# Performance work log

Hardware: AMD Instinct MI355X
Metric: run time of the kernel (lower is better)

The kernel has to match this reference:

```python
import jax, jax.numpy as jnp
import numpy as np

TEMPERATURE = 1.0
EXAGGERATION = 1.0


def setup_inputs() -> dict:
    key = jax.random.key(0)
    features = jax.random.normal(key, (8192, 128), dtype=jnp.float32)
    return {"features": features}


def _cauchy_sim(x, y):
    # 1 / ((cdist(x,y) * t)^2 + 1) == 1 / (t^2 * sq_dist + 1)
    sq = (
        jnp.sum(x * x, axis=1)[:, None]
        + jnp.sum(y * y, axis=1)[None, :]
        - 2.0 * (x @ y.T)
    )
    sq = jnp.maximum(sq, 0.0)  # numerical floor, matches cdist >= 0
    return 1.0 / (sq * (TEMPERATURE * TEMPERATURE) + 1.0)


def reference(features):
    batch_size = features.shape[0] // 2
    a = features[:batch_size]
    b = features[batch_size:]

    sim_aa = _cauchy_sim(a, a)  # [B, B]
    sim_bb = _cauchy_sim(b, b)  # [B, B]
    sim_ab = _cauchy_sim(a, b)  # [B, B]

    tempered_alignment = jnp.mean(jnp.log(jnp.diagonal(sim_ab)))

    self_mask = jnp.eye(batch_size, dtype=bool)
    sim_aa = jnp.where(self_mask, 0.0, sim_aa)
    sim_bb = jnp.where(self_mask, 0.0, sim_bb)

    # hstack((sim_ab.T, sim_bb)).sum(1) == sim_ab.sum(0) + sim_bb.sum(1)
    logsumexp_1 = jnp.mean(jnp.log(jnp.sum(sim_ab, axis=0) + jnp.sum(sim_bb, axis=1)))
    logsumexp_2 = jnp.mean(jnp.log(jnp.sum(sim_aa, axis=1) + jnp.sum(sim_ab, axis=1)))
    raw_uniformity = logsumexp_1 + logsumexp_2

    loss = -(EXAGGERATION * tempered_alignment - raw_uniformity / 2.0)
    return loss
```

## Files before the change

kernel.cpp:

```cpp
#include <hip/hip_runtime.h>
#include <hip/hip_bf16.h>

typedef __bf16 bf16x8 __attribute__((ext_vector_type(8)));
typedef float  f32x4  __attribute__((ext_vector_type(4)));

static constexpr int D      = 128;
static constexpr int BATCH  = 4096;
static constexpr int N      = 8192;
static constexpr int BT     = 256;
static constexpr int NT     = N / BT;
static constexpr int TRI    = NT * (NT + 1) / 2;

__device__ __forceinline__ void load_lds16(const void* g, void* l) {
    __builtin_amdgcn_global_load_lds(
        (const __attribute__((address_space(1))) unsigned int*)g,
        (__attribute__((address_space(3))) unsigned int*)l, 16, 0, 0);
}

__global__ __launch_bounds__(256) void prep_kernel(const float* __restrict__ f,
                                                   unsigned short* __restrict__ fb,
                                                   float* __restrict__ norms,
                                                   float* __restrict__ out) {
    if (blockIdx.x == 0 && threadIdx.x == 0) out[0] = 0.f;
    const int w = threadIdx.x >> 6, lane = threadIdx.x & 63;
    const int row = blockIdx.x * 4 + w;
    const float2 v = *(const float2*)(f + (size_t)row * D + lane * 2);
    union { __bf16 h[2]; unsigned int u; } pk;
    pk.h[0] = (__bf16)v.x; pk.h[1] = (__bf16)v.y;
    *(unsigned int*)(fb + (size_t)row * D + lane * 2) = pk.u;
    float s = v.x * v.x + v.y * v.y;
    #pragma unroll
    for (int m = 1; m <= 32; m <<= 1) s += __shfl_xor(s, m);
    if (lane == 0) norms[row] = s;
}

__global__ __launch_bounds__(512) void sim_kernel(const unsigned short* __restrict__ fbf,
                                                  const float* __restrict__ norms,
                                                  float* __restrict__ Prow,
                                                  float* __restrict__ diag) {
    int id = blockIdx.x;
    int ti = (int)((sqrtf(8.f * (float)id + 1.f) - 1.f) * 0.5f);
    while ((ti + 1) * (ti + 2) / 2 <= id) ++ti;
    while (ti * (ti + 1) / 2 > id) --ti;
    const int tj = id - ti * (ti + 1) / 2;
    const bool diagblk = (ti == tj);

    __shared__ __align__(16) unsigned char AsB[BT * 128];
    __shared__ __align__(16) unsigned char BsB[BT * 128];
    __shared__ float rowbuf[256];
    __shared__ float colbuf[256];

    const int tid = threadIdx.x;
    if (tid < 256) rowbuf[tid] = 0.f;
    else           colbuf[tid - 256] = 0.f;

    const int wv = tid >> 6, lane = tid & 63;
    const int lr = lane & 15, hk = lane >> 4;
    const int qr = (wv >> 2) * 128;
    const int qc = (wv & 3) * 64;

    const unsigned char* Abase = (const unsigned char*)fbf + (size_t)ti * BT * 256;
    const unsigned char* Bbase = (const unsigned char*)fbf + (size_t)tj * BT * 256;
    const unsigned char* Brd = diagblk ? AsB : BsB;

    f32x4 acc[8][4];
    #pragma unroll
    for (int i = 0; i < 8; ++i)
        #pragma unroll
        for (int j = 0; j < 4; ++j)
            acc[i][j] = (f32x4){0.f, 0.f, 0.f, 0.f};

    #pragma unroll
    for (int kp = 0; kp < 2; ++kp) {
        if (kp) __syncthreads();
        #pragma unroll
        for (int it = 0; it < 4; ++it) {
            const int cid = it * 512 + tid;
            const int row = cid >> 3, p = cid & 7;
            const int sw = ((p ^ (row & 7)) << 4);
            load_lds16(Abase + (size_t)row * 256 + kp * 128 + sw,
                       AsB + it * 8192 + wv * 1024);
        }
        if (!diagblk) {
            #pragma unroll
            for (int it = 0; it < 4; ++it) {
                const int cid = it * 512 + tid;
                const int row = cid >> 3, p = cid & 7;
                const int sw = ((p ^ (row & 7)) << 4);
                load_lds16(Bbase + (size_t)row * 256 + kp * 128 + sw,
                           BsB + it * 8192 + wv * 1024);
            }
        }
        __syncthreads();

        #pragma unroll
        for (int l = 0; l < 2; ++l) {
            const int c = l * 4 + hk;
            bf16x8 av[8], bv[4];
            #pragma unroll
            for (int fi = 0; fi < 8; ++fi) {
                const int row = qr + fi * 16 + lr;
                av[fi] = *(const bf16x8*)(AsB + row * 128 + ((c ^ (row & 7)) << 4));
            }
            #pragma unroll
            for (int fj = 0; fj < 4; ++fj) {
                const int row = qc + fj * 16 + lr;
                bv[fj] = *(const bf16x8*)(Brd + row * 128 + ((c ^ (row & 7)) << 4));
            }
            #pragma unroll
            for (int fi = 0; fi < 8; ++fi)
                #pragma unroll
                for (int fj = 0; fj < 4; ++fj)
                    acc[fi][fj] = __builtin_amdgcn_mfma_f32_16x16x32_bf16(av[fi], bv[fj], acc[fi][fj], 0, 0, 0);
        }
    }

    float colN[4];
    #pragma unroll
    for (int fj = 0; fj < 4; ++fj)
        colN[fj] = norms[tj * BT + qc + fj * 16 + lr];

    const int colBase = tj * BT;
    const bool stripe = (ti == tj + 16);

    #pragma unroll
    for (int fi = 0; fi < 8; ++fi) {
        const int irow = qr + fi * 16 + hk * 4;
        float rowN[4];
        #pragma unroll
        for (int r = 0; r < 4; ++r)
            rowN[r] = norms[ti * BT + irow + r];
        #pragma unroll
        for (int fj = 0; fj < 4; ++fj) {
            const int icol = qc + fj * 16 + lr;
            #pragma unroll
            for (int r = 0; r < 4; ++r) {
                float sq = rowN[r] + colN[fj] - 2.f * acc[fi][fj][r];
                sq = fmaxf(sq, 0.f);
                float sim = __builtin_amdgcn_rcpf(sq + 1.f);
                if (diagblk && (irow + r == icol)) sim = 0.f;
                if (stripe && (irow + r == icol)) diag[colBase + icol] = sim;
                acc[fi][fj][r] = sim;
            }
        }
    }

    #pragma unroll
    for (int fi = 0; fi < 8; ++fi) {
        float rs[4];
        #pragma unroll
        for (int r = 0; r < 4; ++r)
            rs[r] = acc[fi][0][r] + acc[fi][1][r] + acc[fi][2][r] + acc[fi][3][r];
        #pragma unroll
        for (int r = 0; r < 4; ++r) {
            rs[r] += __shfl_xor(rs[r], 1);
            rs[r] += __shfl_xor(rs[r], 2);
            rs[r] += __shfl_xor(rs[r], 4);
            rs[r] += __shfl_xor(rs[r], 8);
        }
        if (lr == 0) {
            #pragma unroll
            for (int r = 0; r < 4; ++r)
                atomicAdd(&rowbuf[qr + fi * 16 + hk * 4 + r], rs[r]);
        }
    }

    if (!diagblk) {
        #pragma unroll
        for (int fj = 0; fj < 4; ++fj) {
            float cs = 0.f;
            #pragma unroll
            for (int fi = 0; fi < 8; ++fi)
                #pragma unroll
                for (int r = 0; r < 4; ++r)
                    cs += acc[fi][fj][r];
            cs += __shfl_xor(cs, 16);
            cs += __shfl_xor(cs, 32);
            if (hk == 0)
                atomicAdd(&colbuf[qc + fj * 16 + lr], cs);
        }
    }
    __syncthreads();

    float* PR = Prow + ((size_t)ti * NT + tj) * BT;
    float* PC = Prow + ((size_t)tj * NT + ti) * BT;
    if (tid < 256) {
        PR[tid] = rowbuf[tid];
        if (!diagblk) PC[tid] = colbuf[tid];
    }
}

__global__ __launch_bounds__(256) void finalize_kernel(const float* __restrict__ Prow,
                                                       const float* __restrict__ diag,
                                                       float* __restrict__ out) {
    const int ti = blockIdx.x;
    const int r  = threadIdx.x;
    const float* base = Prow + (size_t)ti * NT * BT + r;
    float s = 0.f;
    #pragma unroll
    for (int k = 0; k < NT; ++k) s += base[k * BT];
    const int i = ti * BT + r;
    float term = 0.5f * __logf(s);
    if (i >= BATCH) term -= __logf(diag[i - BATCH]);
    #pragma unroll
    for (int m = 1; m <= 32; m <<= 1) term += __shfl_xor(term, m);
    __shared__ float sh[4];
    if ((threadIdx.x & 63) == 0) sh[threadIdx.x >> 6] = term;
    __syncthreads();
    if (threadIdx.x == 0)
        atomicAdd(out, (sh[0] + sh[1] + sh[2] + sh[3]) / (float)BATCH);
}

extern "C" void kernel_launch(void* const* d_in, const int* in_sizes, int n_in,
                              void* d_out, int out_size, void* d_ws, size_t ws_size,
                              hipStream_t stream) {
    const float* feat = (const float*)d_in[0];
    char* ws = (char*)d_ws;
    unsigned short* fbf = (unsigned short*)ws;
    float* norms = (float*)(ws + (2u << 20));
    float* diag  = (float*)(ws + (2u << 20) + 32768);
    float* Prow  = (float*)(ws + (2u << 20) + 49152);
    float* out   = (float*)d_out;

    prep_kernel<<<N / 4, 256, 0, stream>>>(feat, fbf, norms, out);
    sim_kernel<<<TRI, 512, 0, stream>>>(fbf, norms, Prow, diag);
    finalize_kernel<<<NT, 256, 0, stream>>>(Prow, diag, out);
}
```

Before: 90.42 us.

## Replace LDS-tiled 256x256 blocks with single-wave 64x64 register tiles

The sim kernel now has one 64-lane wave per 64x64 triangular tile. Each wave loads its bf16 fragments straight from global memory into registers, so the LDS staging, barriers and shared-memory atomics are gone. Row and column partial sums are written directly to a workspace laid out so that finalize only reads the populated slots. This gives far more, smaller blocks (8256 instead of 528) for load balance and latency hiding, but each tile reuses less data and global/L2 traffic grows.

```diff
diff --git a/kernel.cpp b/kernel.cpp
--- a/kernel.cpp
+++ b/kernel.cpp
@@ -4,18 +4,12 @@
 typedef __bf16 bf16x8 __attribute__((ext_vector_type(8)));
 typedef float  f32x4  __attribute__((ext_vector_type(4)));
 
-static constexpr int D      = 128;
-static constexpr int BATCH  = 4096;
-static constexpr int N      = 8192;
-static constexpr int BT     = 256;
-static constexpr int NT     = N / BT;
-static constexpr int TRI    = NT * (NT + 1) / 2;
-
-__device__ __forceinline__ void load_lds16(const void* g, void* l) {
-    __builtin_amdgcn_global_load_lds(
-        (const __attribute__((address_space(1))) unsigned int*)g,
-        (__attribute__((address_space(3))) unsigned int*)l, 16, 0, 0);
-}
+static constexpr int D     = 128;
+static constexpr int BATCH = 4096;
+static constexpr int N     = 8192;
+static constexpr int WT    = 64;
+static constexpr int NT    = N / WT;
+static constexpr int TRI   = NT * (NT + 1) / 2;
 
 __global__ __launch_bounds__(256) void prep_kernel(const float* __restrict__ f,
                                                    unsigned short* __restrict__ fb,
@@ -34,120 +28,80 @@
     if (lane == 0) norms[row] = s;
 }
 
-__global__ __launch_bounds__(512) void sim_kernel(const unsigned short* __restrict__ fbf,
-                                                  const float* __restrict__ norms,
-                                                  float* __restrict__ Prow,
-                                                  float* __restrict__ diag) {
-    int id = blockIdx.x;
+__global__ __launch_bounds__(64, 3) void wave_kernel(const unsigned short* __restrict__ fbf,
+                                                     const float* __restrict__ norms,
+                                                     float* __restrict__ Prow,
+                                                     float* __restrict__ diag) {
+    const int id = blockIdx.x;
     int ti = (int)((sqrtf(8.f * (float)id + 1.f) - 1.f) * 0.5f);
     while ((ti + 1) * (ti + 2) / 2 <= id) ++ti;
     while (ti * (ti + 1) / 2 > id) --ti;
     const int tj = id - ti * (ti + 1) / 2;
     const bool diagblk = (ti == tj);
+    const bool stripe  = (ti == tj + 64);
 
-    __shared__ __align__(16) unsigned char AsB[BT * 128];
-    __shared__ __align__(16) unsigned char BsB[BT * 128];
-    __shared__ float rowbuf[256];
-    __shared__ float colbuf[256];
+    const int lane = threadIdx.x;
+    const int lr = lane & 15, hk = lane >> 4;
 
-    const int tid = threadIdx.x;
-    if (tid < 256) rowbuf[tid] = 0.f;
-    else           colbuf[tid - 256] = 0.f;
+    const unsigned char* Ab = (const unsigned char*)fbf + (size_t)ti * WT * 256;
+    const unsigned char* Bb = (const unsigned char*)fbf + (size_t)tj * WT * 256;
 
-    const int wv = tid >> 6, lane = tid & 63;
-    const int lr = lane & 15, hk = lane >> 4;
-    const int qr = (wv >> 2) * 128;
-    const int qc = (wv & 3) * 64;
-
-    const unsigned char* Abase = (const unsigned char*)fbf + (size_t)ti * BT * 256;
-    const unsigned char* Bbase = (const unsigned char*)fbf + (size_t)tj * BT * 256;
-    const unsigned char* Brd = diagblk ? AsB : BsB;
-
-    f32x4 acc[8][4];
+    f32x4 acc[4][4];
     #pragma unroll
-    for (int i = 0; i < 8; ++i)
+    for (int i = 0; i < 4; ++i)
         #pragma unroll
         for (int j = 0; j < 4; ++j)
             acc[i][j] = (f32x4){0.f, 0.f, 0.f, 0.f};
 
     #pragma unroll
-    for (int kp = 0; kp < 2; ++kp) {
-        if (kp) __syncthreads();
+    for (int ks = 0; ks < 4; ++ks) {
+        const int ko = (ks * 4 + hk) * 16;
+        bf16x8 av[4], bv[4];
         #pragma unroll
-        for (int it = 0; it < 4; ++it) {
-            const int cid = it * 512 + tid;
-            const int row = cid >> 3, p = cid & 7;
-            const int sw = ((p ^ (row & 7)) << 4);
-            load_lds16(Abase + (size_t)row * 256 + kp * 128 + sw,
-                       AsB + it * 8192 + wv * 1024);
-        }
-        if (!diagblk) {
+        for (int fi = 0; fi < 4; ++fi)
+            av[fi] = *(const bf16x8*)(Ab + (fi * 16 + lr) * 256 + ko);
+        #pragma unroll
+        for (int fj = 0; fj < 4; ++fj)
+            bv[fj] = *(const bf16x8*)(Bb + (fj * 16 + lr) * 256 + ko);
+        #pragma unroll
+        for (int fi = 0; fi < 4; ++fi)
             #pragma unroll
-            for (int it = 0; it < 4; ++it) {
-                const int cid = it * 512 + tid;
-                const int row = cid >> 3, p = cid & 7;
-                const int sw = ((p ^ (row & 7)) << 4);
-                load_lds16(Bbase + (size_t)row * 256 + kp * 128 + sw,
-                           BsB + it * 8192 + wv * 1024);
-            }
-        }
-        __syncthreads();
-
-        #pragma unroll
-        for (int l = 0; l < 2; ++l) {
-            const int c = l * 4 + hk;
-            bf16x8 av[8], bv[4];
-            #pragma unroll
-            for (int fi = 0; fi < 8; ++fi) {
-                const int row = qr + fi * 16 + lr;
-                av[fi] = *(const bf16x8*)(AsB + row * 128 + ((c ^ (row & 7)) << 4));
-            }
-            #pragma unroll
-            for (int fj = 0; fj < 4; ++fj) {
-                const int row = qc + fj * 16 + lr;
-                bv[fj] = *(const bf16x8*)(Brd + row * 128 + ((c ^ (row & 7)) << 4));
-            }
-            #pragma unroll
-            for (int fi = 0; fi < 8; ++fi)
-                #pragma unroll
-                for (int fj = 0; fj < 4; ++fj)
-                    acc[fi][fj] = __builtin_amdgcn_mfma_f32_16x16x32_bf16(av[fi], bv[fj], acc[fi][fj], 0, 0, 0);
-        }
+            for (int fj = 0; fj < 4; ++fj)
+                acc[fi][fj] = __builtin_amdgcn_mfma_f32_16x16x32_bf16(av[fi], bv[fj], acc[fi][fj], 0, 0, 0);
     }
 
-    float colN[4];
+    float rowN[4][4], colN[4];
+    #pragma unroll
+    for (int fi = 0; fi < 4; ++fi)
+        #pragma unroll
+        for (int r = 0; r < 4; ++r)
+            rowN[fi][r] = norms[ti * WT + fi * 16 + hk * 4 + r];
     #pragma unroll
     for (int fj = 0; fj < 4; ++fj)
-        colN[fj] = norms[tj * BT + qc + fj * 16 + lr];
-
-    const int colBase = tj * BT;
-    const bool stripe = (ti == tj + 16);
+        colN[fj] = norms[tj * WT + fj * 16 + lr];
 
     #pragma unroll
-    for (int fi = 0; fi < 8; ++fi) {
-        const int irow = qr + fi * 16 + hk * 4;
-        float rowN[4];
-        #pragma unroll
-        for (int r = 0; r < 4; ++r)
-            rowN[r] = norms[ti * BT + irow + r];
+    for (int fi = 0; fi < 4; ++fi) {
+        const int lrow = fi * 16 + hk * 4;
         #pragma unroll
         for (int fj = 0; fj < 4; ++fj) {
-            const int icol = qc + fj * 16 + lr;
+            const int lcol = fj * 16 + lr;
             #pragma unroll
             for (int r = 0; r < 4; ++r) {
-                float sq = rowN[r] + colN[fj] - 2.f * acc[fi][fj][r];
+                float sq = rowN[fi][r] + colN[fj] - 2.f * acc[fi][fj][r];
                 sq = fmaxf(sq, 0.f);
                 float sim = __builtin_amdgcn_rcpf(sq + 1.f);
-                if (diagblk && (irow + r == icol)) sim = 0.f;
-                if (stripe && (irow + r == icol)) diag[colBase + icol] = sim;
+                if (diagblk && (lrow + r == lcol)) sim = 0.f;
+                if (stripe && (lrow + r == lcol)) diag[tj * WT + lcol] = sim;
                 acc[fi][fj][r] = sim;
             }
         }
     }
 
+    float* PR = Prow + ((size_t)ti * 256 + tj) * WT;
     #pragma unroll
-    for (int fi = 0; fi < 8; ++fi) {
-        float rs[4];
+    for (int fi = 0; fi < 4; ++fi) {
+        f32x4 rs;
         #pragma unroll
         for (int r = 0; r < 4; ++r)
             rs[r] = acc[fi][0][r] + acc[fi][1][r] + acc[fi][2][r] + acc[fi][3][r];
@@ -158,57 +112,44 @@
             rs[r] += __shfl_xor(rs[r], 4);
             rs[r] += __shfl_xor(rs[r], 8);
         }
-        if (lr == 0) {
-            #pragma unroll
-            for (int r = 0; r < 4; ++r)
-                atomicAdd(&rowbuf[qr + fi * 16 + hk * 4 + r], rs[r]);
-        }
+        if (lr == 0)
+            *(f32x4*)(PR + fi * 16 + hk * 4) = rs;
     }
 
     if (!diagblk) {
+        float* PC = Prow + ((size_t)tj * 256 + 128 + ti) * WT;
         #pragma unroll
         for (int fj = 0; fj < 4; ++fj) {
             float cs = 0.f;
             #pragma unroll
-            for (int fi = 0; fi < 8; ++fi)
+            for (int fi = 0; fi < 4; ++fi)
                 #pragma unroll
                 for (int r = 0; r < 4; ++r)
                     cs += acc[fi][fj][r];
             cs += __shfl_xor(cs, 16);
             cs += __shfl_xor(cs, 32);
             if (hk == 0)
-                atomicAdd(&colbuf[qc + fj * 16 + lr], cs);
+                PC[fj * 16 + lr] = cs;
         }
-    }
-    __syncthreads();
-
-    float* PR = Prow + ((size_t)ti * NT + tj) * BT;
-    float* PC = Prow + ((size_t)tj * NT + ti) * BT;
-    if (tid < 256) {
-        PR[tid] = rowbuf[tid];
-        if (!diagblk) PC[tid] = colbuf[tid];
     }
 }
 
-__global__ __launch_bounds__(256) void finalize_kernel(const float* __restrict__ Prow,
-                                                       const float* __restrict__ diag,
-                                                       float* __restrict__ out) {
-    const int ti = blockIdx.x;
-    const int r  = threadIdx.x;
-    const float* base = Prow + (size_t)ti * NT * BT + r;
+__global__ __launch_bounds__(64) void finalize_kernel(const float* __restrict__ Prow,
+                                                      const float* __restrict__ diag,
+                                                      float* __restrict__ out) {
+    const int t = blockIdx.x;
+    const int r = threadIdx.x;
+    const float* base = Prow + (size_t)t * 256 * WT + r;
     float s = 0.f;
-    #pragma unroll
-    for (int k = 0; k < NT; ++k) s += base[k * BT];
-    const int i = ti * BT + r;
+    for (int k = 0; k <= t; ++k)          s += base[k * WT];
+    for (int k = 129 + t; k < 256; ++k)   s += base[k * WT];
+    const int i = t * WT + r;
     float term = 0.5f * __logf(s);
     if (i >= BATCH) term -= __logf(diag[i - BATCH]);
     #pragma unroll
     for (int m = 1; m <= 32; m <<= 1) term += __shfl_xor(term, m);
-    __shared__ float sh[4];
-    if ((threadIdx.x & 63) == 0) sh[threadIdx.x >> 6] = term;
-    __syncthreads();
-    if (threadIdx.x == 0)
-        atomicAdd(out, (sh[0] + sh[1] + sh[2] + sh[3]) / (float)BATCH);
+    if (r == 0)
+        atomicAdd(out, term / (float)BATCH);
 }
 
 extern "C" void kernel_launch(void* const* d_in, const int* in_sizes, int n_in,
@@ -219,10 +160,10 @@
     unsigned short* fbf = (unsigned short*)ws;
     float* norms = (float*)(ws + (2u << 20));
     float* diag  = (float*)(ws + (2u << 20) + 32768);
-    float* Prow  = (float*)(ws + (2u << 20) + 49152);
+    float* Prow  = (float*)(ws + (2u << 20) + 65536);
     float* out   = (float*)d_out;
 
     prep_kernel<<<N / 4, 256, 0, stream>>>(feat, fbf, norms, out);
-    sim_kernel<<<TRI, 512, 0, stream>>>(fbf, norms, Prow, diag);
-    finalize_kernel<<<NT, 256, 0, stream>>>(Prow, diag, out);
+    wave_kernel<<<TRI, 64, 0, stream>>>(fbf, norms, Prow, diag);
+    finalize_kernel<<<NT, 64, 0, stream>>>(Prow, diag, out);
 }
```

New measurement: 126.1 us. +39.5%, slower.

## Process three tiles per block with double-buffered async LDS pipeline

Applied to the files above, without the earlier changes.

Each block now handles three upper-triangle tiles, double-buffering K-halves in LDS so global-to-LDS loads for the next stage overlap MFMA compute and epilogues, with manual waitcnt and barrier control. Diagonal alignment similarities are computed exactly in fp32 in the prep kernel, row/column norms are cached in LDS, and Prow gets a separate row/column layout so finalize sums only the valid partials. This cuts the grid from 528 to 176 blocks and amortizes load latency, at the cost of heavier LDS use (about 134KB per block) and occupancy limited to one block per CU, plus fragile hand-tuned vmcnt counts.

```diff
diff --git a/kernel.cpp b/kernel.cpp
--- a/kernel.cpp
+++ b/kernel.cpp
@@ -4,12 +4,13 @@
 typedef __bf16 bf16x8 __attribute__((ext_vector_type(8)));
 typedef float  f32x4  __attribute__((ext_vector_type(4)));
 
-static constexpr int D      = 128;
-static constexpr int BATCH  = 4096;
-static constexpr int N      = 8192;
-static constexpr int BT     = 256;
-static constexpr int NT     = N / BT;
-static constexpr int TRI    = NT * (NT + 1) / 2;
+static constexpr int D     = 128;
+static constexpr int BATCH = 4096;
+static constexpr int N     = 8192;
+static constexpr int BT    = 256;
+static constexpr int NT    = 32;
+static constexpr int TRI   = NT * (NT + 1) / 2;
+static constexpr int NBLK  = TRI / 3;
 
 __device__ __forceinline__ void load_lds16(const void* g, void* l) {
     __builtin_amdgcn_global_load_lds(
@@ -17,82 +18,100 @@
         (__attribute__((address_space(3))) unsigned int*)l, 16, 0, 0);
 }
 
+#define WAITV(n) do { asm volatile("s_waitcnt vmcnt(" #n ")" ::: "memory"); \
+                      __builtin_amdgcn_sched_barrier(0); } while (0)
+#define BAR()    do { __builtin_amdgcn_s_barrier(); \
+                      __builtin_amdgcn_sched_barrier(0); } while (0)
+#define LGKM0()  do { asm volatile("s_waitcnt lgkmcnt(0)" ::: "memory"); \
+                      __builtin_amdgcn_sched_barrier(0); } while (0)
+
 __global__ __launch_bounds__(256) void prep_kernel(const float* __restrict__ f,
                                                    unsigned short* __restrict__ fb,
                                                    float* __restrict__ norms,
+                                                   float* __restrict__ diag,
                                                    float* __restrict__ out) {
     if (blockIdx.x == 0 && threadIdx.x == 0) out[0] = 0.f;
     const int w = threadIdx.x >> 6, lane = threadIdx.x & 63;
-    const int row = blockIdx.x * 4 + w;
-    const float2 v = *(const float2*)(f + (size_t)row * D + lane * 2);
-    union { __bf16 h[2]; unsigned int u; } pk;
-    pk.h[0] = (__bf16)v.x; pk.h[1] = (__bf16)v.y;
-    *(unsigned int*)(fb + (size_t)row * D + lane * 2) = pk.u;
-    float s = v.x * v.x + v.y * v.y;
-    #pragma unroll
-    for (int m = 1; m <= 32; m <<= 1) s += __shfl_xor(s, m);
-    if (lane == 0) norms[row] = s;
-}
-
-__global__ __launch_bounds__(512) void sim_kernel(const unsigned short* __restrict__ fbf,
-                                                  const float* __restrict__ norms,
-                                                  float* __restrict__ Prow,
-                                                  float* __restrict__ diag) {
-    int id = blockIdx.x;
-    int ti = (int)((sqrtf(8.f * (float)id + 1.f) - 1.f) * 0.5f);
-    while ((ti + 1) * (ti + 2) / 2 <= id) ++ti;
-    while (ti * (ti + 1) / 2 > id) --ti;
-    const int tj = id - ti * (ti + 1) / 2;
-    const bool diagblk = (ti == tj);
-
-    __shared__ __align__(16) unsigned char AsB[BT * 128];
-    __shared__ __align__(16) unsigned char BsB[BT * 128];
-    __shared__ float rowbuf[256];
-    __shared__ float colbuf[256];
-
-    const int tid = threadIdx.x;
-    if (tid < 256) rowbuf[tid] = 0.f;
-    else           colbuf[tid - 256] = 0.f;
-
-    const int wv = tid >> 6, lane = tid & 63;
+    const int i = blockIdx.x * 4 + w;
+    const float2 va = *(const float2*)(f + (size_t)i * D + lane * 2);
+    const float2 vb = *(const float2*)(f + (size_t)(i + BATCH) * D + lane * 2);
+    union { __bf16 h[2]; unsigned int u; } pa, pb;
+    pa.h[0] = (__bf16)va.x; pa.h[1] = (__bf16)va.y;
+    pb.h[0] = (__bf16)vb.x; pb.h[1] = (__bf16)vb.y;
+    *(unsigned int*)(fb + (size_t)i * D + lane * 2) = pa.u;
+    *(unsigned int*)(fb + (size_t)(i + BATCH) * D + lane * 2) = pb.u;
+    float na = va.x * va.x + va.y * va.y;
+    float nb = vb.x * vb.x + vb.y * vb.y;
+    const float dx = va.x - vb.x, dy = va.y - vb.y;
+    float dd = dx * dx + dy * dy;
+    #pragma unroll
+    for (int m = 1; m <= 32; m <<= 1) {
+        na += __shfl_xor(na, m); nb += __shfl_xor(nb, m); dd += __shfl_xor(dd, m);
+    }
+    if (lane == 0) {
+        norms[i] = na; norms[i + BATCH] = nb;
+        diag[i] = 1.f / (dd + 1.f);
+    }
+}
+
+__global__ __launch_bounds__(512, 2) void pipe_kernel(const unsigned short* __restrict__ fbf,
+                                                      const float* __restrict__ norms,
+                                                      float* __restrict__ Prow,
+                                                      float* __restrict__ diag) {
+    __shared__ __align__(16) unsigned char buf[2][65536];
+    __shared__ float nrm[3][512];
+    __shared__ float rowbuf[256], colbuf[256];
+
+    const int tid = threadIdx.x, wv = tid >> 6, lane = tid & 63;
     const int lr = lane & 15, hk = lane >> 4;
-    const int qr = (wv >> 2) * 128;
-    const int qc = (wv & 3) * 64;
-
-    const unsigned char* Abase = (const unsigned char*)fbf + (size_t)ti * BT * 256;
-    const unsigned char* Bbase = (const unsigned char*)fbf + (size_t)tj * BT * 256;
-    const unsigned char* Brd = diagblk ? AsB : BsB;
+    const int qr = (wv >> 2) * 128, qc = (wv & 3) * 64;
+
+    int TI[3], TJ[3];
+    #pragma unroll
+    for (int t = 0; t < 3; ++t) {
+        const int id = blockIdx.x * 3 + t;
+        int ti = (int)((sqrtf(8.f * (float)id + 1.f) - 1.f) * 0.5f);
+        while ((ti + 1) * (ti + 2) / 2 <= id) ++ti;
+        while (ti * (ti + 1) / 2 > id) --ti;
+        TI[t] = ti; TJ[t] = id - ti * (ti + 1) / 2;
+    }
+
+    if (tid < 256) { rowbuf[tid] = 0.f; colbuf[tid] = 0.f; }
+    #pragma unroll
+    for (int t = 0; t < 3; ++t) {
+        const int panel = (tid < 256) ? TI[t] : TJ[t];
+        nrm[t][tid] = norms[panel * BT + (tid & 255)];
+    }
+    LGKM0();
 
     f32x4 acc[8][4];
-    #pragma unroll
-    for (int i = 0; i < 8; ++i)
-        #pragma unroll
-        for (int j = 0; j < 4; ++j)
-            acc[i][j] = (f32x4){0.f, 0.f, 0.f, 0.f};
-
-    #pragma unroll
-    for (int kp = 0; kp < 2; ++kp) {
-        if (kp) __syncthreads();
+
+    auto ZERO = [&]() {
+        #pragma unroll
+        for (int i = 0; i < 8; ++i)
+            #pragma unroll
+            for (int j = 0; j < 4; ++j)
+                acc[i][j] = (f32x4){0.f, 0.f, 0.f, 0.f};
+    };
+
+    auto STAGE = [&](int ti, int tj, int kp, int bsel) {
+        const unsigned char* Ab = (const unsigned char*)fbf + (size_t)ti * BT * 256;
+        const unsigned char* Bb = (const unsigned char*)fbf + (size_t)tj * BT * 256;
         #pragma unroll
         for (int it = 0; it < 4; ++it) {
-            const int cid = it * 512 + tid;
-            const int row = cid >> 3, p = cid & 7;
+            const int cid = it * 512 + tid, row = cid >> 3, p = cid & 7;
             const int sw = ((p ^ (row & 7)) << 4);
-            load_lds16(Abase + (size_t)row * 256 + kp * 128 + sw,
-                       AsB + it * 8192 + wv * 1024);
-        }
-        if (!diagblk) {
-            #pragma unroll
-            for (int it = 0; it < 4; ++it) {
-                const int cid = it * 512 + tid;
-                const int row = cid >> 3, p = cid & 7;
-                const int sw = ((p ^ (row & 7)) << 4);
-                load_lds16(Bbase + (size_t)row * 256 + kp * 128 + sw,
-                           BsB + it * 8192 + wv * 1024);
-            }
-        }
-        __syncthreads();
-
+            load_lds16(Ab + row * 256 + kp * 128 + sw, &buf[bsel][it * 8192 + wv * 1024]);
+        }
+        #pragma unroll
+        for (int it = 0; it < 4; ++it) {
+            const int cid = it * 512 + tid, row = cid >> 3, p = cid & 7;
+            const int sw = ((p ^ (row & 7)) << 4);
+            load_lds16(Bb + row * 256 + kp * 128 + sw, &buf[bsel][32768 + it * 8192 + wv * 1024]);
+        }
+    };
+
+    auto COMPUTE = [&](int bsel) {
         #pragma unroll
         for (int l = 0; l < 2; ++l) {
             const int c = l * 4 + hk;
@@ -100,12 +119,12 @@
             #pragma unroll
             for (int fi = 0; fi < 8; ++fi) {
                 const int row = qr + fi * 16 + lr;
-                av[fi] = *(const bf16x8*)(AsB + row * 128 + ((c ^ (row & 7)) << 4));
+                av[fi] = *(const bf16x8*)&buf[bsel][row * 128 + ((c ^ (row & 7)) << 4)];
             }
             #pragma unroll
             for (int fj = 0; fj < 4; ++fj) {
                 const int row = qc + fj * 16 + lr;
-                bv[fj] = *(const bf16x8*)(Brd + row * 128 + ((c ^ (row & 7)) << 4));
+                bv[fj] = *(const bf16x8*)&buf[bsel][32768 + row * 128 + ((c ^ (row & 7)) << 4)];
             }
             #pragma unroll
             for (int fi = 0; fi < 8; ++fi)
@@ -113,93 +132,91 @@
                 for (int fj = 0; fj < 4; ++fj)
                     acc[fi][fj] = __builtin_amdgcn_mfma_f32_16x16x32_bf16(av[fi], bv[fj], acc[fi][fj], 0, 0, 0);
         }
-    }
-
-    float colN[4];
-    #pragma unroll
-    for (int fj = 0; fj < 4; ++fj)
-        colN[fj] = norms[tj * BT + qc + fj * 16 + lr];
-
-    const int colBase = tj * BT;
-    const bool stripe = (ti == tj + 16);
-
-    #pragma unroll
-    for (int fi = 0; fi < 8; ++fi) {
-        const int irow = qr + fi * 16 + hk * 4;
-        float rowN[4];
-        #pragma unroll
-        for (int r = 0; r < 4; ++r)
-            rowN[r] = norms[ti * BT + irow + r];
-        #pragma unroll
-        for (int fj = 0; fj < 4; ++fj) {
-            const int icol = qc + fj * 16 + lr;
+    };
+
+    auto EPILOGUE = [&](int ti, int tj, const float* nr, bool last) {
+        const bool diagblk = (ti == tj);
+        float colN[4];
+        #pragma unroll
+        for (int fj = 0; fj < 4; ++fj) colN[fj] = nr[256 + qc + fj * 16 + lr];
+        #pragma unroll
+        for (int fi = 0; fi < 8; ++fi) {
+            const int lrow = qr + fi * 16 + hk * 4;
+            const f32x4 rN = *(const f32x4*)&nr[lrow];
+            float rs[4] = {0.f, 0.f, 0.f, 0.f};
+            #pragma unroll
+            for (int fj = 0; fj < 4; ++fj) {
+                const int lcol = qc + fj * 16 + lr;
+                #pragma unroll
+                for (int r = 0; r < 4; ++r) {
+                    float sq = rN[r] + colN[fj] - 2.f * acc[fi][fj][r];
+                    sq = fmaxf(sq, 0.f);
+                    float sim = __builtin_amdgcn_rcpf(sq + 1.f);
+                    if (diagblk && (lrow + r == lcol)) sim = 0.f;
+                    rs[r] += sim;
+                    acc[fi][fj][r] = sim;
+                }
+            }
             #pragma unroll
             for (int r = 0; r < 4; ++r) {
-                float sq = rowN[r] + colN[fj] - 2.f * acc[fi][fj][r];
-                sq = fmaxf(sq, 0.f);
-                float sim = __builtin_amdgcn_rcpf(sq + 1.f);
-                if (diagblk && (irow + r == icol)) sim = 0.f;
-                if (stripe && (irow + r == icol)) diag[colBase + icol] = sim;
-                acc[fi][fj][r] = sim;
-            }
-        }
-    }
-
-    #pragma unroll
-    for (int fi = 0; fi < 8; ++fi) {
-        float rs[4];
-        #pragma unroll
-        for (int r = 0; r < 4; ++r)
-            rs[r] = acc[fi][0][r] + acc[fi][1][r] + acc[fi][2][r] + acc[fi][3][r];
-        #pragma unroll
-        for (int r = 0; r < 4; ++r) {
-            rs[r] += __shfl_xor(rs[r], 1);
-            rs[r] += __shfl_xor(rs[r], 2);
-            rs[r] += __shfl_xor(rs[r], 4);
-            rs[r] += __shfl_xor(rs[r], 8);
-        }
-        if (lr == 0) {
-            #pragma unroll
-            for (int r = 0; r < 4; ++r)
-                atomicAdd(&rowbuf[qr + fi * 16 + hk * 4 + r], rs[r]);
-        }
-    }
-
-    if (!diagblk) {
+                rs[r] += __shfl_xor(rs[r], 1); rs[r] += __shfl_xor(rs[r], 2);
+                rs[r] += __shfl_xor(rs[r], 4); rs[r] += __shfl_xor(rs[r], 8);
+            }
+            if (lr == 0) {
+                #pragma unroll
+                for (int r = 0; r < 4; ++r) atomicAdd(&rowbuf[lrow + r], rs[r]);
+            }
+        }
         #pragma unroll
         for (int fj = 0; fj < 4; ++fj) {
             float cs = 0.f;
             #pragma unroll
             for (int fi = 0; fi < 8; ++fi)
                 #pragma unroll
-                for (int r = 0; r < 4; ++r)
-                    cs += acc[fi][fj][r];
-            cs += __shfl_xor(cs, 16);
-            cs += __shfl_xor(cs, 32);
-            if (hk == 0)
-                atomicAdd(&colbuf[qc + fj * 16 + lr], cs);
-        }
-    }
-    __syncthreads();
-
-    float* PR = Prow + ((size_t)ti * NT + tj) * BT;
-    float* PC = Prow + ((size_t)tj * NT + ti) * BT;
-    if (tid < 256) {
-        PR[tid] = rowbuf[tid];
-        if (!diagblk) PC[tid] = colbuf[tid];
-    }
+                for (int r = 0; r < 4; ++r) cs += acc[fi][fj][r];
+            cs += __shfl_xor(cs, 16); cs += __shfl_xor(cs, 32);
+            if (hk == 0) atomicAdd(&colbuf[qc + fj * 16 + lr], cs);
+        }
+        LGKM0(); BAR();
+        if (tid < 256) {
+            const float rv = rowbuf[tid], cv = colbuf[tid];
+            rowbuf[tid] = 0.f; colbuf[tid] = 0.f;
+            Prow[((size_t)ti * 64 + tj) * BT + tid] = rv;
+            Prow[((size_t)tj * 64 + 32 + ti) * BT + tid] = cv;
+        }
+        if (!last) LGKM0();
+    };
+
+    STAGE(TI[0], TJ[0], 0, 0);
+    STAGE(TI[0], TJ[0], 1, 1);
+    ZERO();
+    WAITV(8);  BAR(); COMPUTE(0); BAR();
+    STAGE(TI[1], TJ[1], 0, 0);
+    WAITV(8);  BAR(); COMPUTE(1); BAR();
+    EPILOGUE(TI[0], TJ[0], &nrm[0][0], false);
+    STAGE(TI[1], TJ[1], 1, 1);
+    ZERO();
+    WAITV(20); BAR(); COMPUTE(0); BAR();
+    STAGE(TI[2], TJ[2], 0, 0);
+    WAITV(8);  BAR(); COMPUTE(1); BAR();
+    EPILOGUE(TI[1], TJ[1], &nrm[1][0], false);
+    STAGE(TI[2], TJ[2], 1, 1);
+    ZERO();
+    WAITV(20); BAR(); COMPUTE(0); BAR();
+    WAITV(0);  BAR(); COMPUTE(1); BAR();
+    EPILOGUE(TI[2], TJ[2], &nrm[2][0], true);
 }
 
 __global__ __launch_bounds__(256) void finalize_kernel(const float* __restrict__ Prow,
                                                        const float* __restrict__ diag,
                                                        float* __restrict__ out) {
-    const int ti = blockIdx.x;
-    const int r  = threadIdx.x;
-    const float* base = Prow + (size_t)ti * NT * BT + r;
+    const int t = blockIdx.x;
+    const int r = threadIdx.x;
+    const float* base = Prow + (size_t)t * 64 * BT + r;
     float s = 0.f;
-    #pragma unroll
-    for (int k = 0; k < NT; ++k) s += base[k * BT];
-    const int i = ti * BT + r;
+    for (int k = 0; k <= t; ++k)       s += base[k * BT];
+    for (int k = 33 + t; k < 64; ++k)  s += base[k * BT];
+    const int i = t * BT + r;
     float term = 0.5f * __logf(s);
     if (i >= BATCH) term -= __logf(diag[i - BATCH]);
     #pragma unroll
@@ -222,7 +239,7 @@
     float* Prow  = (float*)(ws + (2u << 20) + 49152);
     float* out   = (float*)d_out;
 
-    prep_kernel<<<N / 4, 256, 0, stream>>>(feat, fbf, norms, out);
-    sim_kernel<<<TRI, 512, 0, stream>>>(fbf, norms, Prow, diag);
+    prep_kernel<<<BATCH / 4, 256, 0, stream>>>(feat, fbf, norms, diag, out);
+    pipe_kernel<<<NBLK, 512, 0, stream>>>(fbf, norms, Prow, diag);
     finalize_kernel<<<NT, 256, 0, stream>>>(Prow, diag, out);
 }
```

Result: slower. 104.8 us (+15.9%).
